# Performance work log

Measured on AMD Instinct MI355X. Metric: run time of the kernel, lower is better.

Reference implementation:

```python
import jax, jax.numpy as jnp
import numpy as np

B, N = 64, 65536  # batch, num point proposals

def setup_inputs() -> dict:
    key = jax.random.key(0)
    k1, k2, k3 = jax.random.split(key, 3)
    pred_logits = jax.random.normal(k1, (B, N, 2), dtype=jnp.float32)
    pred_confusion = jax.random.normal(k2, (B, N, 4), dtype=jnp.float32)
    target_classes = jax.random.randint(k3, (B, N), 0, 2, dtype=jnp.int64)
    return {"pred_logits": pred_logits, "pred_confusion": pred_confusion,
            "target_classes": target_classes}

def reference(pred_logits, pred_confusion, target_classes):
    # argmax over the binary logits per proposal
    src_pred = jnp.argmax(pred_logits, axis=-1)            # [B, N] in {0,1}
    g = target_classes                                     # [B, N] in {0,1}
    # confusion matrix labels: TP=1, FN=2, FP=3, TN=0
    confusion = jnp.where(g == 1,
                          jnp.where(src_pred == 1, 1, 2),
                          jnp.where(src_pred == 1, 3, 0))   # [B, N] int
    # unweighted cross entropy over 4 confusion classes, mean over B*N
    logp = jax.nn.log_softmax(pred_confusion, axis=-1)     # [B, N, 4]
    nll = -jnp.take_along_axis(logp, confusion[..., None], axis=-1)[..., 0]
    return jnp.mean(nll)
```

## Files before the change

### kernel.cpp

```cpp
#include <hip/hip_runtime.h>
#include <hip/hip_bf16.h>


__global__ __launch_bounds__(256) void confusion_nll_kernel(
    const float2* __restrict__ logits,
    const float4* __restrict__ conf,
    const int*    __restrict__ tgt,
    float* __restrict__ out,
    int total)
{
    int idx    = blockIdx.x * blockDim.x + threadIdx.x;
    int stride = gridDim.x * blockDim.x;

    float acc = 0.0f;
    for (int i = idx; i < total; i += stride) {
        float2 l = logits[i];
        float4 c = conf[i];
        int    g = tgt[i];

        int pred = (l.y > l.x) ? 1 : 0;
        int cls = (g == 1) ? (pred ? 1 : 2) : (pred ? 3 : 0);

        float m   = fmaxf(fmaxf(c.x, c.y), fmaxf(c.z, c.w));
        float s   = __expf(c.x - m) + __expf(c.y - m) +
                    __expf(c.z - m) + __expf(c.w - m);
        float lse = m + __logf(s);

        float xc = (cls == 0) ? c.x : (cls == 1) ? c.y : (cls == 2) ? c.z : c.w;
        acc += lse - xc;
    }

    #pragma unroll
    for (int off = 32; off > 0; off >>= 1)
        acc += __shfl_down(acc, off, 64);

    __shared__ float wsum[4];
    int lane = threadIdx.x & 63;
    int wid  = threadIdx.x >> 6;
    if (lane == 0) wsum[wid] = acc;
    __syncthreads();

    if (threadIdx.x == 0) {
        float bsum = wsum[0] + wsum[1] + wsum[2] + wsum[3];
        atomicAdd(out, bsum * (1.0f / (float)total));
    }
}

extern "C" void kernel_launch(void* const* d_in, const int* in_sizes, int n_in,
                              void* d_out, int out_size, void* d_ws, size_t ws_size,
                              hipStream_t stream)
{
    const float2* logits = (const float2*)d_in[0];
    const float4* conf   = (const float4*)d_in[1];
    const int*    tgt    = (const int*)d_in[2];
    float*        out    = (float*)d_out;

    const int total = in_sizes[2];

    hipMemsetAsync(out, 0, out_size * sizeof(float), stream);

    const int block = 256;
    const int grid  = 2048;
    confusion_nll_kernel<<<grid, block, 0, stream>>>(logits, conf, tgt, out, total);
}
```

Baseline: 153.1 us.

## Vectorize loads over four elements and replace atomics with two-pass reduction

Each thread now handles four proposals per iteration: two float4 loads for the logits, four float4 loads for the confusion scores and one int4 load for the targets, which raises bytes per memory instruction. The global atomicAdd and the memset are replaced by per-block partial sums written to workspace, followed by a single-block final reduction kernel. This removes atomic contention and the memset launch but adds a second kernel launch. A scalar tail loop handles totals that are not a multiple of four.

```diff
diff --git a/kernel.cpp b/kernel.cpp
--- a/kernel.cpp
+++ b/kernel.cpp
@@ -2,32 +2,54 @@
 #include <hip/hip_bf16.h>
 
 
-__global__ __launch_bounds__(256) void confusion_nll_kernel(
-    const float2* __restrict__ logits,
+#define NPART 2048
+
+__device__ __forceinline__ float nll_one(float4 c, bool gpos, bool pred)
+{
+    int cls = gpos ? (pred ? 1 : 2) : (pred ? 3 : 0);
+    float m   = fmaxf(fmaxf(c.x, c.y), fmaxf(c.z, c.w));
+    float s   = __expf(c.x - m) + __expf(c.y - m) +
+                __expf(c.z - m) + __expf(c.w - m);
+    float lse = m + __logf(s);
+    float xc  = (cls == 0) ? c.x : (cls == 1) ? c.y : (cls == 2) ? c.z : c.w;
+    return lse - xc;
+}
+
+__global__ __launch_bounds__(256) void confusion_part_kernel(
+    const float4* __restrict__ lg,
     const float4* __restrict__ conf,
-    const int*    __restrict__ tgt,
-    float* __restrict__ out,
+    const int4*   __restrict__ tg,
+    const float2* __restrict__ lg2,
+    const float4* __restrict__ conf1,
+    const int*    __restrict__ tg1,
+    float* __restrict__ partials,
     int total)
 {
-    int idx    = blockIdx.x * blockDim.x + threadIdx.x;
-    int stride = gridDim.x * blockDim.x;
+    const int idx    = blockIdx.x * blockDim.x + threadIdx.x;
+    const int stride = gridDim.x * blockDim.x;
+    const int nvec   = total >> 2;
 
     float acc = 0.0f;
-    for (int i = idx; i < total; i += stride) {
-        float2 l = logits[i];
-        float4 c = conf[i];
-        int    g = tgt[i];
+    for (int v = idx; v < nvec; v += stride) {
+        float4 lA = lg[2 * v];
+        float4 lB = lg[2 * v + 1];
+        float4 c0 = conf[4 * v];
+        float4 c1 = conf[4 * v + 1];
+        float4 c2 = conf[4 * v + 2];
+        float4 c3 = conf[4 * v + 3];
+        int4   g  = tg[v];
 
-        int pred = (l.y > l.x) ? 1 : 0;
-        int cls = (g == 1) ? (pred ? 1 : 2) : (pred ? 3 : 0);
+        acc += nll_one(c0, g.x == 1, lA.y > lA.x);
+        acc += nll_one(c1, g.y == 1, lA.w > lA.z);
+        acc += nll_one(c2, g.z == 1, lB.y > lB.x);
+        acc += nll_one(c3, g.w == 1, lB.w > lB.z);
+    }
 
-        float m   = fmaxf(fmaxf(c.x, c.y), fmaxf(c.z, c.w));
-        float s   = __expf(c.x - m) + __expf(c.y - m) +
-                    __expf(c.z - m) + __expf(c.w - m);
-        float lse = m + __logf(s);
-
-        float xc = (cls == 0) ? c.x : (cls == 1) ? c.y : (cls == 2) ? c.z : c.w;
-        acc += lse - xc;
+    if (blockIdx.x == 0 && threadIdx.x == 0) {
+        for (int i = nvec << 2; i < total; ++i) {
+            float2 l = lg2[i];
+            acc += nll_one(conf1[i], tg1[i] == 1, l.y > l.x);
+        }
     }
 
     #pragma unroll
@@ -40,26 +62,48 @@
     if (lane == 0) wsum[wid] = acc;
     __syncthreads();
 
-    if (threadIdx.x == 0) {
-        float bsum = wsum[0] + wsum[1] + wsum[2] + wsum[3];
-        atomicAdd(out, bsum * (1.0f / (float)total));
-    }
+    if (threadIdx.x == 0)
+        partials[blockIdx.x] = wsum[0] + wsum[1] + wsum[2] + wsum[3];
+}
+
+__global__ __launch_bounds__(256) void confusion_final_kernel(
+    const float* __restrict__ partials, float* __restrict__ out,
+    int npart, float inv_total)
+{
+    float acc = 0.0f;
+    for (int i = threadIdx.x; i < npart; i += 256)
+        acc += partials[i];
+
+    #pragma unroll
+    for (int off = 32; off > 0; off >>= 1)
+        acc += __shfl_down(acc, off, 64);
+
+    __shared__ float wsum[4];
+    int lane = threadIdx.x & 63;
+    int wid  = threadIdx.x >> 6;
+    if (lane == 0) wsum[wid] = acc;
+    __syncthreads();
+
+    if (threadIdx.x == 0)
+        out[0] = (wsum[0] + wsum[1] + wsum[2] + wsum[3]) * inv_total;
 }
 
 extern "C" void kernel_launch(void* const* d_in, const int* in_sizes, int n_in,
                               void* d_out, int out_size, void* d_ws, size_t ws_size,
                               hipStream_t stream)
 {
-    const float2* logits = (const float2*)d_in[0];
-    const float4* conf   = (const float4*)d_in[1];
-    const int*    tgt    = (const int*)d_in[2];
-    float*        out    = (float*)d_out;
+    const float4* lg    = (const float4*)d_in[0];
+    const float4* conf  = (const float4*)d_in[1];
+    const int4*   tg    = (const int4*)d_in[2];
+    const float2* lg2   = (const float2*)d_in[0];
+    const int*    tg1   = (const int*)d_in[2];
+    float*        out   = (float*)d_out;
+    float*        parts = (float*)d_ws;
 
     const int total = in_sizes[2];
 
-    hipMemsetAsync(out, 0, out_size * sizeof(float), stream);
-
-    const int block = 256;
-    const int grid  = 2048;
-    confusion_nll_kernel<<<grid, block, 0, stream>>>(logits, conf, tgt, out, total);
+    confusion_part_kernel<<<NPART, 256, 0, stream>>>(
+        lg, conf, tg, lg2, conf, tg1, parts, total);
+    confusion_final_kernel<<<1, 256, 0, stream>>>(
+        parts, out, NPART, 1.0f / (float)total);
 }
```

After: 136.7 us. 10.7% less time.
